# Kernel tuning notes

Hardware: AMD Instinct MI355X
Metric: run time of the kernel (lower is better)

Reference implementation:

```python
import jax, jax.numpy as jnp
import numpy as np

N = 100000          # nodes
E = 3_200_000       # edges (avg degree 32)
F_IN = 1433
H1, C1 = 8, 8       # conv1: 8 heads x 8 channels -> 64 concat
H2, C2 = 1, 7       # conv2: 1 head x 7 classes
NEG_SLOPE = 0.2


def setup_inputs() -> dict:
    key = jax.random.key(0)
    ks = jax.random.split(key, 10)
    x = jax.random.normal(ks[0], (N, F_IN), dtype=jnp.float32)
    edge_index = jax.random.randint(ks[1], (2, E), 0, N, dtype=jnp.int64)
    s1 = 1.0 / np.sqrt(F_IN)
    s2 = 1.0 / np.sqrt(H1 * C1)
    return {
        "x": x,
        "edge_index": edge_index,
        "W1": jax.random.normal(ks[2], (F_IN, H1 * C1), dtype=jnp.float32) * s1,
        "att_src1": jax.random.normal(ks[3], (H1, C1), dtype=jnp.float32) * s2,
        "att_dst1": jax.random.normal(ks[4], (H1, C1), dtype=jnp.float32) * s2,
        "b1": jnp.zeros((H1 * C1,), dtype=jnp.float32),
        "W2": jax.random.normal(ks[5], (H1 * C1, H2 * C2), dtype=jnp.float32) * s2,
        "att_src2": jax.random.normal(ks[6], (H2, C2), dtype=jnp.float32),
        "att_dst2": jax.random.normal(ks[7], (H2, C2), dtype=jnp.float32),
        "b2": jnp.zeros((H2 * C2,), dtype=jnp.float32),
    }


def gat_conv(x, src, dst, W, att_src, att_dst, b, heads, ch):
    # x: [N, F_in]; src/dst: [E'] (self-loops already appended)
    h = (x @ W).reshape(N, heads, ch)                     # [N, H, C]
    a_src = jnp.einsum('nhc,hc->nh', h, att_src)          # [N, H]
    a_dst = jnp.einsum('nhc,hc->nh', h, att_dst)
    e = a_src[src] + a_dst[dst]                           # [E', H]
    e = jax.nn.leaky_relu(e, NEG_SLOPE)
    # segment softmax over incoming edges of each dst node
    m = jax.ops.segment_max(e, dst, num_segments=N)       # [N, H]
    w = jnp.exp(e - m[dst])
    denom = jax.ops.segment_sum(w, dst, num_segments=N)   # [N, H]
    alpha = w / denom[dst]                                # [E', H]
    msg = alpha[:, :, None] * h[src]                      # [E', H, C]
    out = jax.ops.segment_sum(msg, dst, num_segments=N)   # [N, H, C]
    return out.reshape(N, heads * ch) + b


def reference(x, edge_index, W1, att_src1, att_dst1, b1, W2, att_src2, att_dst2, b2):
    loops = jnp.arange(N, dtype=edge_index.dtype)
    src = jnp.concatenate([edge_index[0], loops])
    dst = jnp.concatenate([edge_index[1], loops])
    # eval mode: all dropout layers are identity
    h = gat_conv(x, src, dst, W1, att_src1, att_dst1, b1, H1, C1)   # [N, 64]
    h = jax.nn.elu(h)
    h = gat_conv(h, src, dst, W2, att_src2, att_dst2, b2, H2, C2)   # [N, 7]
    return jax.nn.log_softmax(h, axis=1)
```

## Files before the change

kernel.cpp:

```cpp
#include <hip/hip_runtime.h>
#include <hip/hip_bf16.h>
#include <math.h>

#define NN 100000
#define EE 3200000
#define ET (EE + NN)
#define FIN 1433
#define KPAD 1440
#define NT 45
#define F1 64
#define F2 7
#define G1B 782
#define CAP 128
#define BINS 200
#define SB1 256
#define CH_E 12891
#define NB4 196
#define A1B 3125

typedef __attribute__((ext_vector_type(8))) short short8;
typedef __attribute__((ext_vector_type(4))) float f32x4;
typedef __attribute__((address_space(3))) unsigned int u32_lds;
typedef __attribute__((address_space(1))) const unsigned int u32_glb;

static __device__ __forceinline__ unsigned short f2bf(float f) {
  __hip_bfloat16 h = __float2bfloat16(f);
  return *reinterpret_cast<unsigned short*>(&h);
}
static __device__ __forceinline__ float bf2f(unsigned short u) {
  return __uint_as_float((unsigned int)u << 16);
}

__global__ __launch_bounds__(256) void k_prep(const float* __restrict__ W1,
                                              unsigned short* __restrict__ WT) {
  int i = blockIdx.x * 256 + threadIdx.x;
  if (i < F1 * KPAD) {
    int c = i / KPAD, k = i - c * KPAD;
    WT[i] = f2bf((k < FIN) ? W1[k * F1 + c] : 0.f);
  }
}

#define BM 128
#define TILEA 16384
#define TILEB 4096
#define BUFB (TILEA + TILEB)

__global__ __launch_bounds__(256) void k_fuse1(const float* __restrict__ X,
                                               const unsigned short* __restrict__ WT,
                                               unsigned short* __restrict__ Hb,
                                               const int* __restrict__ ei,
                                               int* __restrict__ histM) {
  if (blockIdx.x >= G1B) {
    __shared__ int hist[BINS];
    const int b = blockIdx.x - G1B;
    for (int i = threadIdx.x; i < BINS; i += 256) hist[i] = 0;
    __syncthreads();
    const int e0 = b * CH_E, e1 = min(e0 + CH_E, ET);
    for (int e = e0 + threadIdx.x; e < e1; e += 256) {
      int dst = (e < EE) ? ei[EE + e] : (e - EE);
      atomicAdd(&hist[dst >> 9], 1);
    }
    __syncthreads();
    for (int i = threadIdx.x; i < BINS; i += 256) histM[b * BINS + i] = hist[i];
    return;
  }
  __shared__ __align__(16) char smem[2 * BUFB];
  const int tid = threadIdx.x;
  const int lane = tid & 63;
  const int wid = tid >> 6;
  const int row0 = blockIdx.x * BM;
  const int wr = (wid >> 1) * 64;
  const int wc = (wid & 1) * 32;
  const int l15 = lane & 15, l4 = lane >> 4;

  const int lrq = tid >> 3;
  const int mq = tid & 7;
  const char* Xb = (const char*)X;
  size_t aoff[4];
#pragma unroll
  for (int q = 0; q < 4; ++q) {
    int lr = q * 32 + lrq;
    int gr = row0 + lr; if (gr >= NN) gr = NN - 1;
    int c = mq ^ (lr & 7);
    aoff[q] = (size_t)gr * (FIN * 4) + (size_t)c * 16;
  }
  const unsigned short* bsrc =
      WT + (tid >> 2) * KPAD + (((tid & 3) ^ ((tid >> 3) & 3)) << 3);

  f32x4 acc[4][2];
#pragma unroll
  for (int a = 0; a < 4; ++a)
#pragma unroll
    for (int b = 0; b < 2; ++b) acc[a][b] = 0.f;

  auto gstage = [&](int k0, char* buf) {
#pragma unroll
    for (int q = 0; q < 4; ++q) {
      __builtin_amdgcn_global_load_lds(
          (u32_glb*)(Xb + aoff[q] + (size_t)k0 * 4),
          (u32_lds*)(buf + q * 4096 + wid * 1024), 16, 0, 0);
    }
  };

  gstage(0, smem);
  {
    short8 b0 = *(const short8*)(bsrc + 0);
    *(short8*)(smem + TILEA + tid * 16) = b0;
  }
  __syncthreads();

  int cur = 0;
  for (int t = 0; t < NT; ++t) {
    char* buf = smem + cur * BUFB;
    char* nbuf = smem + (cur ^ 1) * BUFB;
    const bool have_next = (t + 1 < NT);
    const bool tail = (t + 1 == NT - 1);
    short8 bnext;
    f32x4 atail[4];
    if (have_next) {
      if (!tail) {
        gstage((t + 1) * 32, nbuf);
      } else {
#pragma unroll
        for (int q = 0; q < 4; ++q) {
          int lr = q * 32 + lrq;
          int gr = row0 + lr; if (gr >= NN) gr = NN - 1;
          int c = mq ^ (lr & 7);
          int kb = (NT - 1) * 32 + c * 4;
          const float* xp = X + (size_t)gr * FIN + kb;
#pragma unroll
          for (int j = 0; j < 4; ++j)
            atail[q][j] = (kb + j < FIN) ? xp[j] : 0.f;
        }
      }
      bnext = *(const short8*)(bsrc + (t + 1) * 32);
    }

    short8 af[4], bf[2];
    const int sz = l15 & 7;
#pragma unroll
    for (int fr = 0; fr < 4; ++fr) {
      int r = wr + fr * 16 + l15;
      f32x4 a0 = *(const f32x4*)(buf + r * 128 + ((2 * l4) ^ sz) * 16);
      f32x4 a1 = *(const f32x4*)(buf + r * 128 + ((2 * l4 + 1) ^ sz) * 16);
      short8 v;
#pragma unroll
      for (int j = 0; j < 4; ++j) {
        v[j] = (short)f2bf(a0[j]);
        v[4 + j] = (short)f2bf(a1[j]);
      }
      af[fr] = v;
    }
#pragma unroll
    for (int fc = 0; fc < 2; ++fc) {
      int c = wc + fc * 16 + l15;
      int jp = l4 ^ ((c >> 1) & 3);
      bf[fc] = *(const short8*)(buf + TILEA + c * 64 + jp * 16);
    }
#pragma unroll
    for (int fr = 0; fr < 4; ++fr)
#pragma unroll
      for (int fc = 0; fc < 2; ++fc)
        acc[fr][fc] = __builtin_amdgcn_mfma_f32_16x16x32_bf16(
            af[fr], bf[fc], acc[fr][fc], 0, 0, 0);

    if (have_next) {
      if (tail) {
#pragma unroll
        for (int q = 0; q < 4; ++q)
          *(f32x4*)(nbuf + (q * 32 + lrq) * 128 + mq * 16) = atail[q];
      }
      *(short8*)(nbuf + TILEA + tid * 16) = bnext;
    }
    __syncthreads();
    cur ^= 1;
  }

#pragma unroll
  for (int fr = 0; fr < 4; ++fr) {
    int rbase = row0 + wr + fr * 16 + l4 * 4;
#pragma unroll
    for (int q = 0; q < 4; ++q) {
      int r = rbase + q;
      if (r < NN) {
#pragma unroll
        for (int fc = 0; fc < 2; ++fc)
          Hb[(size_t)r * F1 + wc + fc * 16 + l15] = f2bf(acc[fr][fc][q]);
      }
    }
  }
}

__global__ __launch_bounds__(256) void k_scanM(int* __restrict__ histM,
                                               int* __restrict__ binS,
                                               int* __restrict__ binE) {
  __shared__ int s[256];
  const int t = threadIdx.x;
  int total = 0;
  if (t < BINS)
    for (int b = 0; b < SB1; ++b) total += histM[b * BINS + t];
  s[t] = total;
  __syncthreads();
  for (int off = 1; off < 256; off <<= 1) {
    int v = s[t];
    int u = (t >= off) ? s[t - off] : 0;
    __syncthreads();
    s[t] = v + u;
    __syncthreads();
  }
  if (t < BINS) {
    int run = s[t] - total;
    binS[t] = run;
    for (int b = 0; b < SB1; ++b) {
      int h = histM[b * BINS + t];
      histM[b * BINS + t] = run;
      run += h;
    }
    binE[t] = run;
  }
}

__global__ __launch_bounds__(256) void k_bin(const int* __restrict__ ei,
                                             const int* __restrict__ histM,
                                             unsigned int* __restrict__ binned) {
  __shared__ int cur[BINS];
  const int b = blockIdx.x;
  for (int i = threadIdx.x; i < BINS; i += 256) cur[i] = histM[b * BINS + i];
  __syncthreads();
  const int e0 = b * CH_E, e1 = min(e0 + CH_E, ET);
  for (int e = e0 + threadIdx.x; e < e1; e += 256) {
    int dst = (e < EE) ? ei[EE + e] : (e - EE);
    int src = (e < EE) ? ei[e] : dst;
    int pos = atomicAdd(&cur[dst >> 9], 1);
    binned[pos] = ((unsigned)(dst & 511) << 17) | (unsigned)src;
  }
}

__global__ __launch_bounds__(256) void k_fuse2(const unsigned short* __restrict__ Hb,
                                               const float* __restrict__ attS,
                                               const float* __restrict__ attD,
                                               float* __restrict__ aS,
                                               float* __restrict__ aD,
                                               const unsigned int* __restrict__ binned,
                                               const int* __restrict__ binS,
                                               const int* __restrict__ binE,
                                               int* __restrict__ cnt,
                                               int* __restrict__ csr) {
  if (blockIdx.x >= A1B) {
    __shared__ int lcnt[512];
    const int g = blockIdx.x - A1B;
    for (int i = threadIdx.x; i < 512; i += 256) lcnt[i] = 0;
    __syncthreads();
    const int s0 = binS[g], s1 = binE[g];
    const int nbase = g << 9;
    for (int i = s0 + threadIdx.x; i < s1; i += 256) {
      unsigned v = binned[i];
      int ld = v >> 17;
      int src = (int)(v & 0x1FFFFu);
      int pos = atomicAdd(&lcnt[ld], 1);
      csr[((size_t)(nbase + ld) << 7) + pos] = src;
    }
    __syncthreads();
    for (int i = threadIdx.x; i < 512; i += 256) {
      int n = nbase + i;
      if (n < NN) cnt[n] = lcnt[i];
    }
    return;
  }
  __shared__ float s_s[64], s_d[64];
  if (threadIdx.x < 64) { s_s[threadIdx.x] = attS[threadIdx.x]; s_d[threadIdx.x] = attD[threadIdx.x]; }
  __syncthreads();
  int idx = blockIdx.x * 256 + threadIdx.x;
  int n = idx >> 3, h = idx & 7;
  if (n >= NN) return;
  short8 v8 = *(const short8*)(Hb + (size_t)n * 64 + h * 8);
  float ss = 0.f, dd = 0.f;
#pragma unroll
  for (int c = 0; c < 8; ++c) {
    float v = bf2f((unsigned short)v8[c]);
    ss = fmaf(v, s_s[h * 8 + c], ss);
    dd = fmaf(v, s_d[h * 8 + c], dd);
  }
  aS[n * 8 + h] = ss;
  aD[n * 8 + h] = dd;
}

__global__ __launch_bounds__(256) void k_agg1(const unsigned short* __restrict__ Hb,
                                              const float* __restrict__ aS,
                                              const float* __restrict__ aD,
                                              const int* __restrict__ cnt,
                                              const int* __restrict__ csr,
                                              const float* __restrict__ b1,
                                              const float* __restrict__ W2,
                                              const float* __restrict__ s2,
                                              const float* __restrict__ d2,
                                              unsigned short* __restrict__ H2b,
                                              float* __restrict__ aD2) {
  __shared__ float s_w2[448];
  __shared__ float s_ss[7], s_dd[7];
  __shared__ float s_b1[64];
  for (int i = threadIdx.x; i < 448; i += 256) s_w2[i] = W2[i];
  if (threadIdx.x < 7) { s_ss[threadIdx.x] = s2[threadIdx.x]; s_dd[threadIdx.x] = d2[threadIdx.x]; }
  if (threadIdx.x < 64) s_b1[threadIdx.x] = b1[threadIdx.x];
  __syncthreads();

  const int wv = threadIdx.x >> 6, lane = threadIdx.x & 63;
  const int n = blockIdx.x * 4 + wv;
  if (n >= NN) return;
  const int eg = lane >> 3, q = lane & 7;
  const float adv = aD[n * 8 + q];
  const int beg = n << 7;
  const int deg = cnt[n];
  float acc[8] = {};
  float den = 0.f;
#pragma unroll 2
  for (int i = eg; i < deg; i += 8) {
    int s = csr[beg + i];
    float e = aS[s * 8 + q] + adv;
    e = (e > 0.f) ? e : 0.2f * e;
    float w = __expf(e);
    den += w;
    short8 hv = *(const short8*)(Hb + (size_t)s * 64 + q * 8);
#pragma unroll
    for (int c = 0; c < 8; ++c)
      acc[c] = fmaf(w, bf2f((unsigned short)hv[c]), acc[c]);
  }
#pragma unroll
  for (int off = 8; off < 64; off <<= 1) {
    den += __shfl_xor(den, off, 64);
#pragma unroll
    for (int c = 0; c < 8; ++c) acc[c] += __shfl_xor(acc[c], off, 64);
  }
  if (eg == 0) {
    float inv = 1.f / den;
    float v[8];
#pragma unroll
    for (int c = 0; c < 8; ++c) {
      float t = acc[c] * inv + s_b1[q * 8 + c];
      v[c] = (t > 0.f) ? t : (__expf(t) - 1.f);
    }
    float p[7] = {};
#pragma unroll
    for (int c = 0; c < 8; ++c) {
      const float* wr = &s_w2[(q * 8 + c) * 7];
#pragma unroll
      for (int j = 0; j < 7; ++j) p[j] = fmaf(v[c], wr[j], p[j]);
    }
#pragma unroll
    for (int off = 1; off < 8; off <<= 1) {
#pragma unroll
      for (int j = 0; j < 7; ++j) p[j] += __shfl_xor(p[j], off, 64);
    }
    if (q == 0) {
      float s = 0.f, d = 0.f;
      short8 row;
#pragma unroll
      for (int j = 0; j < 7; ++j) {
        row[j] = (short)f2bf(p[j]);
        s = fmaf(p[j], s_ss[j], s);
        d = fmaf(p[j], s_dd[j], d);
      }
      row[7] = (short)f2bf(s);
      *(short8*)(H2b + (size_t)n * 8) = row;
      aD2[n] = d;
    }
  }
}

__global__ __launch_bounds__(256) void k_agg2(const unsigned short* __restrict__ H2b,
                                              const float* __restrict__ aD2,
                                              const int* __restrict__ cnt,
                                              const int* __restrict__ csr,
                                              const float* __restrict__ b2,
                                              float* __restrict__ out) {
  const int wv = threadIdx.x >> 6, lane = threadIdx.x & 63;
  const int n = blockIdx.x * 4 + wv;
  if (n >= NN) return;
  const float adv = aD2[n];
  const int beg = n << 7;
  const int deg = cnt[n];
  float acc[7] = {};
  float den = 0.f;
  for (int j = lane; j < deg; j += 64) {
    int s = csr[beg + j];
    short8 hv = *(const short8*)(H2b + (size_t)s * 8);
    float e = bf2f((unsigned short)hv[7]) + adv;
    e = (e > 0.f) ? e : 0.2f * e;
    float wgt = __expf(e);
    den += wgt;
#pragma unroll
    for (int c = 0; c < 7; ++c)
      acc[c] = fmaf(wgt, bf2f((unsigned short)hv[c]), acc[c]);
  }
#pragma unroll
  for (int off = 32; off > 0; off >>= 1) {
    den += __shfl_xor(den, off, 64);
#pragma unroll
    for (int c = 0; c < 7; ++c) acc[c] += __shfl_xor(acc[c], off, 64);
  }
  if (lane == 0) {
    float inv = 1.f / den;
    float v[7];
    float m = -1e30f;
#pragma unroll
    for (int c = 0; c < 7; ++c) { v[c] = acc[c] * inv + b2[c]; m = fmaxf(m, v[c]); }
    float se = 0.f;
#pragma unroll
    for (int c = 0; c < 7; ++c) se += __expf(v[c] - m);
    float lse = m + __logf(se);
#pragma unroll
    for (int c = 0; c < 7; ++c) out[n * 7 + c] = v[c] - lse;
  }
}

extern "C" void kernel_launch(void* const* d_in, const int* in_sizes, int n_in,
                              void* d_out, int out_size, void* d_ws, size_t ws_size,
                              hipStream_t stream) {
  const float* x   = (const float*)d_in[0];
  const int*   ei  = (const int*)d_in[1];
  const float* W1  = (const float*)d_in[2];
  const float* as1 = (const float*)d_in[3];
  const float* ad1 = (const float*)d_in[4];
  const float* b1  = (const float*)d_in[5];
  const float* W2  = (const float*)d_in[6];
  const float* as2 = (const float*)d_in[7];
  const float* ad2 = (const float*)d_in[8];
  const float* b2  = (const float*)d_in[9];
  float* out = (float*)d_out;

  char* ws = (char*)d_ws;
  size_t off = 0;
  auto alloc = [&](size_t bytes) {
    void* p = ws + off;
    off += (bytes + 255) & ~(size_t)255;
    return p;
  };
  unsigned short* h1b = (unsigned short*)alloc((size_t)NN * 64 * 2);
  float* sc1    = (float*)alloc((size_t)NN * 8 * 4);
  float* dc1    = (float*)alloc((size_t)NN * 8 * 4);
  unsigned short* h2b = (unsigned short*)alloc((size_t)NN * 8 * 2);
  float* dc2    = (float*)alloc((size_t)NN * 4);
  int*   cnt    = (int*)alloc((size_t)NN * 4);
  int*   csr    = (int*)alloc((size_t)NN * CAP * 4);
  int*   histM  = (int*)alloc((size_t)SB1 * BINS * 4);
  int*   binS   = (int*)alloc((size_t)BINS * 4);
  int*   binE   = (int*)alloc((size_t)BINS * 4);
  unsigned int* binned = (unsigned int*)alloc((size_t)ET * 4);
  unsigned short* w1t = (unsigned short*)alloc((size_t)F1 * KPAD * 2);

  k_prep<<<(F1 * KPAD + 255) / 256, 256, 0, stream>>>(W1, w1t);

  k_fuse1<<<G1B + SB1, 256, 0, stream>>>(x, w1t, h1b, ei, histM);

  k_scanM<<<1, 256, 0, stream>>>(histM, binS, binE);

  k_bin<<<SB1, 256, 0, stream>>>(ei, histM, binned);

  k_fuse2<<<A1B + NB4, 256, 0, stream>>>(h1b, as1, ad1, sc1, dc1,
                                         binned, binS, binE, cnt, csr);

  k_agg1<<<(NN + 3) / 4, 256, 0, stream>>>(h1b, sc1, dc1, cnt, csr, b1,
                                           W2, as2, ad2, h2b, dc2);

  k_agg2<<<(NN + 3) / 4, 256, 0, stream>>>(h2b, dc2, cnt, csr, b2, out);
}
```

Baseline: 436.7 us.

## Halve GEMM row tile to 64 and give each wave all 64 columns

The first-layer X@W1 GEMM tile shrinks from 128 to 64 rows per block, which doubles the number of GEMM blocks. Each wave now owns 16 rows across all 64 output columns instead of a 64x32 sub-tile. The aim is more blocks in flight and a smaller LDS footprint per block, for better occupancy and latency hiding on this memory-bound GEMM. In exchange, W1 tiles are reloaded twice as often and each wave does fewer MFMAs per LDS read, so there is less reuse.

```diff
diff --git a/kernel.cpp b/kernel.cpp
--- a/kernel.cpp
+++ b/kernel.cpp
@@ -10,7 +10,7 @@
 #define NT 45
 #define F1 64
 #define F2 7
-#define G1B 782
+#define G1B 1563
 #define CAP 128
 #define BINS 200
 #define SB1 256
@@ -40,8 +40,8 @@
   }
 }
 
-#define BM 128
-#define TILEA 16384
+#define BM 64
+#define TILEA 8192
 #define TILEB 4096
 #define BUFB (TILEA + TILEB)
 
@@ -69,16 +69,14 @@
   const int lane = tid & 63;
   const int wid = tid >> 6;
   const int row0 = blockIdx.x * BM;
-  const int wr = (wid >> 1) * 64;
-  const int wc = (wid & 1) * 32;
   const int l15 = lane & 15, l4 = lane >> 4;
 
   const int lrq = tid >> 3;
   const int mq = tid & 7;
   const char* Xb = (const char*)X;
-  size_t aoff[4];
-#pragma unroll
-  for (int q = 0; q < 4; ++q) {
+  size_t aoff[2];
+#pragma unroll
+  for (int q = 0; q < 2; ++q) {
     int lr = q * 32 + lrq;
     int gr = row0 + lr; if (gr >= NN) gr = NN - 1;
     int c = mq ^ (lr & 7);
@@ -87,15 +85,13 @@
   const unsigned short* bsrc =
       WT + (tid >> 2) * KPAD + (((tid & 3) ^ ((tid >> 3) & 3)) << 3);
 
-  f32x4 acc[4][2];
-#pragma unroll
-  for (int a = 0; a < 4; ++a)
-#pragma unroll
-    for (int b = 0; b < 2; ++b) acc[a][b] = 0.f;
+  f32x4 acc[4];
+#pragma unroll
+  for (int fc = 0; fc < 4; ++fc) acc[fc] = 0.f;
 
   auto gstage = [&](int k0, char* buf) {
 #pragma unroll
-    for (int q = 0; q < 4; ++q) {
+    for (int q = 0; q < 2; ++q) {
       __builtin_amdgcn_global_load_lds(
           (u32_glb*)(Xb + aoff[q] + (size_t)k0 * 4),
           (u32_lds*)(buf + q * 4096 + wid * 1024), 16, 0, 0);
@@ -116,13 +112,13 @@
     const bool have_next = (t + 1 < NT);
     const bool tail = (t + 1 == NT - 1);
     short8 bnext;
-    f32x4 atail[4];
+    f32x4 atail[2];
     if (have_next) {
       if (!tail) {
         gstage((t + 1) * 32, nbuf);
       } else {
 #pragma unroll
-        for (int q = 0; q < 4; ++q) {
+        for (int q = 0; q < 2; ++q) {
           int lr = q * 32 + lrq;
           int gr = row0 + lr; if (gr >= NN) gr = NN - 1;
           int c = mq ^ (lr & 7);
@@ -136,38 +132,30 @@
       bnext = *(const short8*)(bsrc + (t + 1) * 32);
     }
 
-    short8 af[4], bf[2];
-    const int sz = l15 & 7;
-#pragma unroll
-    for (int fr = 0; fr < 4; ++fr) {
-      int r = wr + fr * 16 + l15;
+    short8 a;
+    {
+      const int r = wid * 16 + l15;
+      const int sz = l15 & 7;
       f32x4 a0 = *(const f32x4*)(buf + r * 128 + ((2 * l4) ^ sz) * 16);
       f32x4 a1 = *(const f32x4*)(buf + r * 128 + ((2 * l4 + 1) ^ sz) * 16);
-      short8 v;
 #pragma unroll
       for (int j = 0; j < 4; ++j) {
-        v[j] = (short)f2bf(a0[j]);
-        v[4 + j] = (short)f2bf(a1[j]);
+        a[j] = (short)f2bf(a0[j]);
+        a[4 + j] = (short)f2bf(a1[j]);
       }
-      af[fr] = v;
-    }
-#pragma unroll
-    for (int fc = 0; fc < 2; ++fc) {
-      int c = wc + fc * 16 + l15;
+    }
+#pragma unroll
+    for (int fc = 0; fc < 4; ++fc) {
+      int c = fc * 16 + l15;
       int jp = l4 ^ ((c >> 1) & 3);
-      bf[fc] = *(const short8*)(buf + TILEA + c * 64 + jp * 16);
-    }
-#pragma unroll
-    for (int fr = 0; fr < 4; ++fr)
-#pragma unroll
-      for (int fc = 0; fc < 2; ++fc)
-        acc[fr][fc] = __builtin_amdgcn_mfma_f32_16x16x32_bf16(
-            af[fr], bf[fc], acc[fr][fc], 0, 0, 0);
+      short8 b = *(const short8*)(buf + TILEA + c * 64 + jp * 16);
+      acc[fc] = __builtin_amdgcn_mfma_f32_16x16x32_bf16(a, b, acc[fc], 0, 0, 0);
+    }
 
     if (have_next) {
       if (tail) {
 #pragma unroll
-        for (int q = 0; q < 4; ++q)
+        for (int q = 0; q < 2; ++q)
           *(f32x4*)(nbuf + (q * 32 + lrq) * 128 + mq * 16) = atail[q];
       }
       *(short8*)(nbuf + TILEA + tid * 16) = bnext;
@@ -176,17 +164,14 @@
     cur ^= 1;
   }
 
-#pragma unroll
-  for (int fr = 0; fr < 4; ++fr) {
-    int rbase = row0 + wr + fr * 16 + l4 * 4;
-#pragma unroll
-    for (int q = 0; q < 4; ++q) {
-      int r = rbase + q;
-      if (r < NN) {
-#pragma unroll
-        for (int fc = 0; fc < 2; ++fc)
-          Hb[(size_t)r * F1 + wc + fc * 16 + l15] = f2bf(acc[fr][fc][q]);
-      }
+  const int rbase = row0 + wid * 16 + l4 * 4;
+#pragma unroll
+  for (int j = 0; j < 4; ++j) {
+    int r = rbase + j;
+    if (r < NN) {
+#pragma unroll
+      for (int fc = 0; fc < 4; ++fc)
+        Hb[(size_t)r * F1 + fc * 16 + l15] = f2bf(acc[fc][j]);
     }
   }
 }
```

New measurement: 420.1 us, median of 2. -3.8%, faster.
